# Kernel tuning notes

Hardware: AMD Instinct MI355X
Metric: run time of the kernel (lower is better)

## Reference

```python
import jax, jax.numpy as jnp
import numpy as np

DIM = 4096
N_HEADS = 32
N_KV_HEADS = 8
HEAD_DIM = DIM // N_HEADS  # 128
N_REP = N_HEADS // N_KV_HEADS  # 4
B, S = 1, 2048
ROPE_THETA = 500000.0


def setup_inputs() -> dict:
    key = jax.random.key(0)
    ks = jax.random.split(key, 5)
    sc = 0.02
    x = jax.random.normal(ks[0], (B, S, DIM), jnp.float32)
    wq = jax.random.normal(ks[1], (DIM, N_HEADS * HEAD_DIM), jnp.float32) * sc
    wk = jax.random.normal(ks[2], (DIM, N_KV_HEADS * HEAD_DIM), jnp.float32) * sc
    wv = jax.random.normal(ks[3], (DIM, N_KV_HEADS * HEAD_DIM), jnp.float32) * sc
    wo = jax.random.normal(ks[4], (N_HEADS * HEAD_DIM, DIM), jnp.float32) * sc
    # rotary frequencies: freqs_cis = exp(i * t * theta^(-2j/d)), j in [0, head_dim/2)
    inv_freq = 1.0 / (ROPE_THETA ** (jnp.arange(0, HEAD_DIM, 2, dtype=jnp.float32) / HEAD_DIM))
    t = jnp.arange(S, dtype=jnp.float32)
    ang = jnp.outer(t, inv_freq)  # (S, head_dim/2)
    freqs_cos = jnp.cos(ang)
    freqs_sin = jnp.sin(ang)
    # additive causal mask, broadcastable to (B, H, S, S)
    mask = jnp.where(jnp.triu(jnp.ones((S, S), bool), k=1), -jnp.inf, 0.0).astype(jnp.float32)[None, None]
    return {"x": x, "wq": wq, "wk": wk, "wv": wv, "wo": wo,
            "freqs_cos": freqs_cos, "freqs_sin": freqs_sin, "mask": mask}


def _apply_rotary(t, cos, sin):
    # t: (B, S, n, hd); complex multiply on consecutive pairs (x0,x1),(x2,x3),...
    b, s, n, hd = t.shape
    tr = t.reshape(b, s, n, hd // 2, 2)
    re, im = tr[..., 0], tr[..., 1]
    c = cos[None, :, None, :]
    sn = sin[None, :, None, :]
    out_re = re * c - im * sn
    out_im = re * sn + im * c
    return jnp.stack([out_re, out_im], axis=-1).reshape(b, s, n, hd)


def reference(x, wq, wk, wv, wo, freqs_cos, freqs_sin, mask):
    b, s, _ = x.shape
    xq = (x @ wq).reshape(b, s, N_HEADS, HEAD_DIM)
    xk = (x @ wk).reshape(b, s, N_KV_HEADS, HEAD_DIM)
    xv = (x @ wv).reshape(b, s, N_KV_HEADS, HEAD_DIM)
    xq = _apply_rotary(xq, freqs_cos, freqs_sin)
    xk = _apply_rotary(xk, freqs_cos, freqs_sin)
    # repeat_kv (GQA): expand kv heads to match query heads
    keys = jnp.repeat(xk, N_REP, axis=2)    # (b, s, H, hd)
    values = jnp.repeat(xv, N_REP, axis=2)
    # (b, H, s, hd)
    q = xq.transpose(0, 2, 1, 3)
    k = keys.transpose(0, 2, 1, 3)
    v = values.transpose(0, 2, 1, 3)
    scores = jnp.einsum('bhqd,bhkd->bhqk', q, k) / np.sqrt(HEAD_DIM).astype(np.float32)
    scores = scores + mask
    probs = jax.nn.softmax(scores.astype(jnp.float32), axis=-1).astype(q.dtype)
    out = jnp.einsum('bhqk,bhkd->bhqd', probs, v)
    out = out.transpose(0, 2, 1, 3).reshape(b, s, N_HEADS * HEAD_DIM)
    return out @ wo
```

## Files before the change

kernel.cpp:

```cpp
#include <hip/hip_runtime.h>
#include <cstdint>
#include <cstddef>

typedef _Float16 f16_t;
typedef f16_t f16x8 __attribute__((ext_vector_type(8)));
typedef float  floatx4 __attribute__((ext_vector_type(4)));

#define S_LEN 2048
#define DIM_  4096
#define NH    32
#define NKV   8
#define HD    128
#define KV_DIM (NKV * HD)
#define QLD   (DIM_ + 2 * KV_DIM)

__device__ __forceinline__ float bf16r(float x) {
    uint32_t u = __float_as_uint(x);
    u = (u + 0x7fffu + ((u >> 16) & 1u)) & 0xffff0000u;
    return __uint_as_float(u);
}

__device__ __forceinline__ void gload_lds16(const f16_t* g, f16_t* l) {
    __builtin_amdgcn_global_load_lds(
        (const __attribute__((address_space(1))) void*)g,
        (__attribute__((address_space(3))) void*)l, 16, 0, 0);
}

__global__ void f32_to_f16_kernel(const float* __restrict__ in,
                                  f16_t* __restrict__ out, int n) {
    int i = (blockIdx.x * blockDim.x + threadIdx.x) * 8;
    if (i >= n) return;
    float4 a = *(const float4*)(in + i);
    float4 b = *(const float4*)(in + i + 4);
    f16x8 o;
    o[0] = (f16_t)bf16r(a.x); o[1] = (f16_t)bf16r(a.y);
    o[2] = (f16_t)bf16r(a.z); o[3] = (f16_t)bf16r(a.w);
    o[4] = (f16_t)bf16r(b.x); o[5] = (f16_t)bf16r(b.y);
    o[6] = (f16_t)bf16r(b.z); o[7] = (f16_t)bf16r(b.w);
    *(f16x8*)(out + i) = o;
}

__global__ void transpose_weights_kernel(const float* __restrict__ wq,
                                         const float* __restrict__ wk,
                                         const float* __restrict__ wv,
                                         const float* __restrict__ wo,
                                         f16_t* __restrict__ wqkvT,
                                         f16_t* __restrict__ woT) {
    __shared__ float tile[32][33];
    int bid = blockIdx.x;
    const float* in; f16_t* out; int C;
    if (bid < 16384)      { in = wq; out = wqkvT;                          C = 4096; }
    else if (bid < 20480) { bid -= 16384; in = wk; out = wqkvT + (size_t)4096 * 4096; C = 1024; }
    else if (bid < 24576) { bid -= 20480; in = wv; out = wqkvT + (size_t)5120 * 4096; C = 1024; }
    else                  { bid -= 24576; in = wo; out = woT;              C = 4096; }
    int gpr = C / 32;
    int bx = (bid % gpr) * 32;
    int by = (bid / gpr) * 32;
    int tx = threadIdx.x, ty = threadIdx.y;
#pragma unroll
    for (int i = 0; i < 4; i++) {
        int r = ty + i * 8;
        tile[r][tx] = in[(size_t)(by + r) * C + bx + tx];
    }
    __syncthreads();
#pragma unroll
    for (int i = 0; i < 4; i++) {
        int r = ty + i * 8;
        out[(size_t)(bx + r) * 4096 + by + tx] = (f16_t)bf16r(tile[tx][r]);
    }
}

__global__ void transpose_f16_kernel(const f16_t* __restrict__ in,
                                     f16_t* __restrict__ out,
                                     int ldi, int ldo) {
    __shared__ float tile[32][33];
    int bx = blockIdx.x * 32;
    int by = blockIdx.y * 32;
    int tx = threadIdx.x, ty = threadIdx.y;
#pragma unroll
    for (int i = 0; i < 4; i++) {
        int r = ty + i * 8;
        tile[r][tx] = (float)in[(size_t)(by + r) * ldi + bx + tx];
    }
    __syncthreads();
#pragma unroll
    for (int i = 0; i < 4; i++) {
        int r = ty + i * 8;
        out[(size_t)(bx + r) * ldo + by + tx] = (f16_t)tile[tx][r];
    }
}

template <typename OutT>
__global__ __launch_bounds__(256) void gemm_bt_kernel(
        const f16_t* __restrict__ A, const f16_t* __restrict__ BT,
        OutT* __restrict__ C, int M, int N, int K) {
    constexpr int BM = 128, BN = 128, BK = 32;
    __shared__ f16_t As[BM * BK];
    __shared__ f16_t Bs[BN * BK];

    const int tid  = threadIdx.x;
    const int lane = tid & 63;
    const int wave = tid >> 6;
    const int wm = (wave >> 1) * 64;
    const int wn = (wave & 1) * 64;
    const int quad = lane >> 4;
    const int l16  = lane & 15;
    const int m0 = blockIdx.y * BM;
    const int n0 = blockIdx.x * BN;

    const int sr  = tid >> 2;
    const int sc8 = (tid & 3) * 8;
    const f16_t* Ag = A  + (size_t)(m0 + sr) * K + sc8;
    const f16_t* Bg = BT + (size_t)(n0 + sr) * K + sc8;
    f16_t* AsW0 = &As[sr * BK + sc8];
    f16_t* AsW1 = &As[(sr + 64) * BK + sc8];
    f16_t* BsW0 = &Bs[sr * BK + sc8];
    f16_t* BsW1 = &Bs[(sr + 64) * BK + sc8];

    floatx4 acc[4][4] = {};

    for (int k0 = 0; k0 < K; k0 += BK) {
        gload_lds16(Ag + k0, AsW0);
        gload_lds16(Ag + k0 + (size_t)64 * K, AsW1);
        gload_lds16(Bg + k0, BsW0);
        gload_lds16(Bg + k0 + (size_t)64 * K, BsW1);
        asm volatile("s_waitcnt vmcnt(0)" ::: "memory");
        __syncthreads();

        f16x8 af[4], bfr[4];
#pragma unroll
        for (int mt = 0; mt < 4; mt++)
            af[mt] = *(const f16x8*)&As[(wm + mt * 16 + l16) * BK + quad * 8];
#pragma unroll
        for (int nt = 0; nt < 4; nt++)
            bfr[nt] = *(const f16x8*)&Bs[(wn + nt * 16 + l16) * BK + quad * 8];
#pragma unroll
        for (int mt = 0; mt < 4; mt++)
#pragma unroll
            for (int nt = 0; nt < 4; nt++)
                acc[mt][nt] = __builtin_amdgcn_mfma_f32_16x16x32_f16(
                    af[mt], bfr[nt], acc[mt][nt], 0, 0, 0);
        __syncthreads();
    }

#pragma unroll
    for (int mt = 0; mt < 4; mt++)
#pragma unroll
        for (int nt = 0; nt < 4; nt++)
#pragma unroll
            for (int rg = 0; rg < 4; rg++) {
                int row = m0 + wm + mt * 16 + quad * 4 + rg;
                int col = n0 + wn + nt * 16 + l16;
                C[(size_t)row * N + col] = (OutT)acc[mt][nt][rg];
            }
}

__global__ __launch_bounds__(512) void attn_kernel(
        const f16_t* __restrict__ QKV, const f16_t* __restrict__ Vt,
        const float* __restrict__ fcos, const float* __restrict__ fsin,
        f16_t* __restrict__ O) {
    constexpr int BK = 64;
    constexpr int KS = HD + 8;
    constexpr int VS = BK + 8;
    __shared__ f16_t Ks[BK][KS];
    __shared__ f16_t Vs[HD][VS];
    __shared__ f16_t Ps[8][16][72];

    const int tid  = threadIdx.x;
    const int lane = tid & 63;
    const int wave = tid >> 6;
    const int quad = lane >> 4;
    const int l16  = lane & 15;

    const int bid = blockIdx.x;
    const int h   = bid & 31;
    const int g   = bid >> 5;
    const int qt  = (g < 8) ? g : 23 - g;
    const int q0  = qt * 128;
    const int hkv = h >> 2;

    const int qrow = q0 + wave * 16 + l16;
    f16x8 qf[4];
    {
        const f16_t* Qg = QKV + (size_t)qrow * QLD + h * HD;
        const float* cr = fcos + qrow * 64;
        const float* sr = fsin + qrow * 64;
#pragma unroll
        for (int c = 0; c < 4; c++) {
            f16x8 v = *(const f16x8*)(Qg + c * 32 + quad * 8);
#pragma unroll
            for (int u = 0; u < 4; u++) {
                int fi = c * 16 + quad * 4 + u;
                float cc = bf16r(cr[fi]), ss = bf16r(sr[fi]);
                float re = (float)v[2 * u], im = (float)v[2 * u + 1];
                v[2 * u]     = (f16_t)(re * cc - im * ss);
                v[2 * u + 1] = (f16_t)(re * ss + im * cc);
            }
            qf[c] = v;
        }
    }

    floatx4 o_acc[8] = {};
    float m_run[4], l_run[4];
#pragma unroll
    for (int i = 0; i < 4; i++) { m_run[i] = -1e30f; l_run[i] = 0.f; }
    const float scale = 0.08838834764831845f;

    const int q_lo = q0 + wave * 16;
    const int q_hi = q_lo + 15;
    const int ntiles = q0 / BK + 2;

    const int krr = tid >> 4;
    const int kcc = (tid & 15) * 8;
    const int vr  = tid >> 3;
    const int vc  = (tid & 7) * 8;
    const f16_t* Vg = Vt + (size_t)hkv * HD * S_LEN;

    for (int t = 0; t < ntiles; t++) {
        const int k0 = t * BK;

#pragma unroll
        for (int p = 0; p < 2; p++) {
            int krow = k0 + p * 32 + krr;
            f16x8 v = *(const f16x8*)(QKV + (size_t)krow * QLD + DIM_ + hkv * HD + kcc);
            const float* cr = fcos + krow * 64;
            const float* sr = fsin + krow * 64;
#pragma unroll
            for (int u = 0; u < 4; u++) {
                int fi = kcc / 2 + u;
                float cc = bf16r(cr[fi]), ss = bf16r(sr[fi]);
                float re = (float)v[2 * u], im = (float)v[2 * u + 1];
                v[2 * u]     = (f16_t)(re * cc - im * ss);
                v[2 * u + 1] = (f16_t)(re * ss + im * cc);
            }
            *(f16x8*)&Ks[p * 32 + krr][kcc] = v;
        }
#pragma unroll
        for (int p = 0; p < 2; p++)
            *(f16x8*)&Vs[p * 64 + vr][vc] =
                *(const f16x8*)(Vg + (size_t)(p * 64 + vr) * S_LEN + k0 + vc);
        __syncthreads();

        if (k0 <= q_hi) {
            floatx4 sc4[4] = {};
#pragma unroll
            for (int nt = 0; nt < 4; nt++)
#pragma unroll
                for (int ks = 0; ks < 4; ks++) {
                    f16x8 kf = *(const f16x8*)&Ks[nt * 16 + l16][ks * 32 + quad * 8];
                    sc4[nt] = __builtin_amdgcn_mfma_f32_16x16x32_f16(qf[ks], kf, sc4[nt], 0, 0, 0);
                }

            const bool needmask = (k0 + BK - 1) > q_lo;
#pragma unroll
            for (int nt = 0; nt < 4; nt++)
#pragma unroll
                for (int rg = 0; rg < 4; rg++) {
                    float s = sc4[nt][rg] * scale;
                    if (needmask) {
                        int qg = q_lo + quad * 4 + rg;
                        int kg = k0 + nt * 16 + l16;
                        if (kg > qg) s = -1e30f;
                    }
                    sc4[nt][rg] = s;
                }

            float alpha[4];
#pragma unroll
            for (int rg = 0; rg < 4; rg++) {
                float m = fmaxf(fmaxf(sc4[0][rg], sc4[1][rg]), fmaxf(sc4[2][rg], sc4[3][rg]));
#pragma unroll
                for (int off = 8; off >= 1; off >>= 1)
                    m = fmaxf(m, __shfl_xor(m, off, 64));
                float mn = fmaxf(m_run[rg], m);
                alpha[rg] = __expf(m_run[rg] - mn);
                m_run[rg] = mn;
            }
            float rsum[4] = {0.f, 0.f, 0.f, 0.f};
#pragma unroll
            for (int nt = 0; nt < 4; nt++)
#pragma unroll
                for (int rg = 0; rg < 4; rg++) {
                    float p = __expf(sc4[nt][rg] - m_run[rg]);
                    sc4[nt][rg] = p;
                    rsum[rg] += p;
                }
#pragma unroll
            for (int rg = 0; rg < 4; rg++) {
                float s = rsum[rg];
#pragma unroll
                for (int off = 8; off >= 1; off >>= 1)
                    s += __shfl_xor(s, off, 64);
                l_run[rg] = l_run[rg] * alpha[rg] + s;
            }
#pragma unroll
            for (int dt = 0; dt < 8; dt++)
#pragma unroll
                for (int rg = 0; rg < 4; rg++) o_acc[dt][rg] *= alpha[rg];

#pragma unroll
            for (int nt = 0; nt < 4; nt++)
#pragma unroll
                for (int rg = 0; rg < 4; rg++)
                    Ps[wave][quad * 4 + rg][nt * 16 + l16] = (f16_t)sc4[nt][rg];
            asm volatile("s_waitcnt lgkmcnt(0)" ::: "memory");
            __builtin_amdgcn_sched_barrier(0);

#pragma unroll
            for (int ks = 0; ks < 2; ks++) {
                f16x8 pf = *(const f16x8*)&Ps[wave][l16][ks * 32 + quad * 8];
#pragma unroll
                for (int dt = 0; dt < 8; dt++) {
                    f16x8 vf = *(const f16x8*)&Vs[dt * 16 + l16][ks * 32 + quad * 8];
                    o_acc[dt] = __builtin_amdgcn_mfma_f32_16x16x32_f16(pf, vf, o_acc[dt], 0, 0, 0);
                }
            }
        }
        __syncthreads();
    }

#pragma unroll
    for (int rg = 0; rg < 4; rg++) {
        float inv_l = 1.0f / l_run[rg];
#pragma unroll
        for (int dt = 0; dt < 8; dt++) {
            int row = q0 + wave * 16 + quad * 4 + rg;
            int col = h * HD + dt * 16 + l16;
            O[(size_t)row * (NH * HD) + col] = (f16_t)(o_acc[dt][rg] * inv_l);
        }
    }
}

extern "C" void kernel_launch(void* const* d_in, const int* in_sizes, int n_in,
                              void* d_out, int out_size, void* d_ws, size_t ws_size,
                              hipStream_t stream) {
    const float* x    = (const float*)d_in[0];
    const float* wq   = (const float*)d_in[1];
    const float* wk   = (const float*)d_in[2];
    const float* wv   = (const float*)d_in[3];
    const float* wo   = (const float*)d_in[4];
    const float* fcos = (const float*)d_in[5];
    const float* fsin = (const float*)d_in[6];
    float* out = (float*)d_out;

    char* ws = (char*)d_ws;
    constexpr size_t MB = 1024 * 1024;
    f16_t* xb    = (f16_t*)(ws + 0 * MB);
    f16_t* wqkvT = (f16_t*)(ws + 16 * MB);
    f16_t* woT   = (f16_t*)(ws + 64 * MB);
    f16_t* QKVb  = (f16_t*)(ws + 96 * MB);
    f16_t* Vt    = (f16_t*)(ws + 120 * MB);
    f16_t* attnb = (f16_t*)(ws + 124 * MB);

    f32_to_f16_kernel<<<S_LEN * DIM_ / 8 / 256, 256, 0, stream>>>(x, xb, S_LEN * DIM_);
    transpose_weights_kernel<<<40960, dim3(32, 8), 0, stream>>>(wq, wk, wv, wo, wqkvT, woT);

    gemm_bt_kernel<f16_t><<<dim3(QLD / 128, S_LEN / 128), 256, 0, stream>>>(
        xb, wqkvT, QKVb, S_LEN, QLD, DIM_);

    transpose_f16_kernel<<<dim3(KV_DIM / 32, S_LEN / 32), dim3(32, 8), 0, stream>>>(
        QKVb + 5120, Vt, QLD, S_LEN);

    attn_kernel<<<512, 512, 0, stream>>>(QKVb, Vt, fcos, fsin, attnb);

    gemm_bt_kernel<float><<<dim3(DIM_ / 128, S_LEN / 128), 256, 0, stream>>>(
        attnb, woT, out, S_LEN, DIM_, DIM_);
}
```

Baseline: 602.2 us.

## Replace GEMM with triple-buffered swizzled-LDS pipelined kernel and larger tiles

```diff
diff --git a/kernel.cpp b/kernel.cpp
--- a/kernel.cpp
+++ b/kernel.cpp
@@ -90,63 +90,114 @@
     }
 }
 
-template <typename OutT>
-__global__ __launch_bounds__(256) void gemm_bt_kernel(
+template <int BM, int BN, typename OutT>
+__global__ __launch_bounds__(512) void gemm_pipe_kernel(
         const f16_t* __restrict__ A, const f16_t* __restrict__ BT,
-        OutT* __restrict__ C, int M, int N, int K) {
-    constexpr int BM = 128, BN = 128, BK = 32;
-    __shared__ f16_t As[BM * BK];
-    __shared__ f16_t Bs[BN * BK];
+        OutT* __restrict__ C, int M, int N, int K, int nbx) {
+    constexpr int BK = 32;
+    constexpr int WN = BN / 64;
+    constexpr int WM = 8 / WN;
+    constexpr int MT = BM / WM / 16;
+    constexpr int NT = 4;
+    constexpr int ABY = BM * BK * 2;
+    constexpr int BBY = BN * BK * 2;
+    constexpr int AISS = ABY / 8192;
+    constexpr int BISS = BBY / 8192;
+    constexpr int LOADS = AISS + BISS;
+    constexpr int BUF_EL = (ABY + BBY) / 2;
+
+    __shared__ f16_t lds[3 * BUF_EL];
 
     const int tid  = threadIdx.x;
     const int lane = tid & 63;
     const int wave = tid >> 6;
-    const int wm = (wave >> 1) * 64;
-    const int wn = (wave & 1) * 64;
     const int quad = lane >> 4;
     const int l16  = lane & 15;
-    const int m0 = blockIdx.y * BM;
-    const int n0 = blockIdx.x * BN;
-
-    const int sr  = tid >> 2;
-    const int sc8 = (tid & 3) * 8;
-    const f16_t* Ag = A  + (size_t)(m0 + sr) * K + sc8;
-    const f16_t* Bg = BT + (size_t)(n0 + sr) * K + sc8;
-    f16_t* AsW0 = &As[sr * BK + sc8];
-    f16_t* AsW1 = &As[(sr + 64) * BK + sc8];
-    f16_t* BsW0 = &Bs[sr * BK + sc8];
-    f16_t* BsW1 = &Bs[(sr + 64) * BK + sc8];
-
-    floatx4 acc[4][4] = {};
-
-    for (int k0 = 0; k0 < K; k0 += BK) {
-        gload_lds16(Ag + k0, AsW0);
-        gload_lds16(Ag + k0 + (size_t)64 * K, AsW1);
-        gload_lds16(Bg + k0, BsW0);
-        gload_lds16(Bg + k0 + (size_t)64 * K, BsW1);
-        asm volatile("s_waitcnt vmcnt(0)" ::: "memory");
-        __syncthreads();
-
-        f16x8 af[4], bfr[4];
-#pragma unroll
-        for (int mt = 0; mt < 4; mt++)
-            af[mt] = *(const f16x8*)&As[(wm + mt * 16 + l16) * BK + quad * 8];
-#pragma unroll
-        for (int nt = 0; nt < 4; nt++)
-            bfr[nt] = *(const f16x8*)&Bs[(wn + nt * 16 + l16) * BK + quad * 8];
-#pragma unroll
-        for (int mt = 0; mt < 4; mt++)
-#pragma unroll
-            for (int nt = 0; nt < 4; nt++)
+    const int wn = (wave % WN) * 64;
+    const int wm = (wave / WN) * (BM / WM);
+
+    const int nwg = gridDim.x;
+    const int swz = (blockIdx.x & 7) * (nwg >> 3) + (blockIdx.x >> 3);
+    const int m0 = (swz / nbx) * BM;
+    const int n0 = (swz % nbx) * BN;
+
+    const f16_t* Arow = A  + (size_t)m0 * K;
+    const f16_t* Brow = BT + (size_t)n0 * K;
+    const int nt_tiles = K / BK;
+
+    floatx4 acc[MT][NT] = {};
+
+    auto stage = [&](int t, int q) {
+        const int k0 = t * BK;
+        f16_t* LdA = lds + q * BUF_EL;
+#pragma unroll
+        for (int j = 0; j < AISS; j++) {
+            int Lb  = j * 8192 + tid * 16;
+            int row = Lb >> 6;
+            int cb  = (Lb & 48) ^ (((Lb >> 7) & 3) << 4);
+            gload_lds16(Arow + (size_t)row * K + k0 + (cb >> 1), LdA + (Lb >> 1));
+        }
+        f16_t* LdB = lds + q * BUF_EL + ABY / 2;
+#pragma unroll
+        for (int j = 0; j < BISS; j++) {
+            int Lb  = j * 8192 + tid * 16;
+            int row = Lb >> 6;
+            int cb  = (Lb & 48) ^ (((Lb >> 7) & 3) << 4);
+            gload_lds16(Brow + (size_t)row * K + k0 + (cb >> 1), LdB + (Lb >> 1));
+        }
+    };
+
+    stage(0, 0);
+    stage(1, 1);
+    if constexpr (LOADS == 4) asm volatile("s_waitcnt vmcnt(4)" ::: "memory");
+    else                      asm volatile("s_waitcnt vmcnt(3)" ::: "memory");
+    __builtin_amdgcn_s_barrier();
+    __builtin_amdgcn_sched_barrier(0);
+
+    for (int t = 0; t < nt_tiles; ++t) {
+        const int cur = t % 3;
+        const bool pre = (t + 2 < nt_tiles);
+        if (pre) stage(t + 2, (t + 2) % 3);
+
+        const f16_t* Ab = lds + cur * BUF_EL;
+        const f16_t* Bb = Ab + ABY / 2;
+        f16x8 af[MT], bf[NT];
+#pragma unroll
+        for (int mt = 0; mt < MT; mt++) {
+            int r  = wm + mt * 16 + l16;
+            int cb = (quad * 16) ^ (((r >> 1) & 3) << 4);
+            af[mt] = *(const f16x8*)(Ab + r * 32 + (cb >> 1));
+        }
+#pragma unroll
+        for (int nt = 0; nt < NT; nt++) {
+            int r  = wn + nt * 16 + l16;
+            int cb = (quad * 16) ^ (((r >> 1) & 3) << 4);
+            bf[nt] = *(const f16x8*)(Bb + r * 32 + (cb >> 1));
+        }
+        asm volatile("s_waitcnt lgkmcnt(0)" ::: "memory");
+        __builtin_amdgcn_sched_barrier(0);
+        __builtin_amdgcn_s_setprio(1);
+#pragma unroll
+        for (int mt = 0; mt < MT; mt++)
+#pragma unroll
+            for (int nt = 0; nt < NT; nt++)
                 acc[mt][nt] = __builtin_amdgcn_mfma_f32_16x16x32_f16(
-                    af[mt], bfr[nt], acc[mt][nt], 0, 0, 0);
-        __syncthreads();
-    }
-
-#pragma unroll
-    for (int mt = 0; mt < 4; mt++)
-#pragma unroll
-        for (int nt = 0; nt < 4; nt++)
+                    af[mt], bf[nt], acc[mt][nt], 0, 0, 0);
+        __builtin_amdgcn_s_setprio(0);
+        if (pre) {
+            if constexpr (LOADS == 4) asm volatile("s_waitcnt vmcnt(4)" ::: "memory");
+            else                      asm volatile("s_waitcnt vmcnt(3)" ::: "memory");
+        } else {
+            asm volatile("s_waitcnt vmcnt(0)" ::: "memory");
+        }
+        __builtin_amdgcn_s_barrier();
+        __builtin_amdgcn_sched_barrier(0);
+    }
+
+#pragma unroll
+    for (int mt = 0; mt < MT; mt++)
+#pragma unroll
+        for (int nt = 0; nt < NT; nt++)
 #pragma unroll
             for (int rg = 0; rg < 4; rg++) {
                 int row = m0 + wm + mt * 16 + quad * 4 + rg;
@@ -355,14 +406,14 @@
     f32_to_f16_kernel<<<S_LEN * DIM_ / 8 / 256, 256, 0, stream>>>(x, xb, S_LEN * DIM_);
     transpose_weights_kernel<<<40960, dim3(32, 8), 0, stream>>>(wq, wk, wv, wo, wqkvT, woT);
 
-    gemm_bt_kernel<f16_t><<<dim3(QLD / 128, S_LEN / 128), 256, 0, stream>>>(
-        xb, wqkvT, QKVb, S_LEN, QLD, DIM_);
+    gemm_pipe_kernel<256, 256, f16_t><<<192, 512, 0, stream>>>(
+        xb, wqkvT, QKVb, S_LEN, QLD, DIM_, QLD / 256);
 
     transpose_f16_kernel<<<dim3(KV_DIM / 32, S_LEN / 32), dim3(32, 8), 0, stream>>>(
         QKVb + 5120, Vt, QLD, S_LEN);
 
     attn_kernel<<<512, 512, 0, stream>>>(QKVb, Vt, fcos, fsin, attnb);
 
-    gemm_bt_kernel<float><<<dim3(DIM_ / 128, S_LEN / 128), 256, 0, stream>>>(
-        attnb, woT, out, S_LEN, DIM_, DIM_);
-}
+    gemm_pipe_kernel<256, 128, float><<<256, 512, 0, stream>>>(
+        attnb, woT, out, S_LEN, DIM_, DIM_, DIM_ / 128);
+}
```

New measurement: 561.9 us. 1.07x faster.
